# Performance work log

Measured on AMD Instinct MI355X. Metric: run time of the kernel, lower is better.

## Reference

```python
import jax, jax.numpy as jnp
import numpy as np

B, C_IN, C_OUT, H, W, K = 8, 64, 64, 128, 128, 3
KK = K * K


def _conv(x, w, b):
    # 3x3, stride 1, padding 1 (matches nn.Conv2d(stride=1, padding=1))
    y = jax.lax.conv_general_dilated(
        x, w, window_strides=(1, 1), padding=((1, 1), (1, 1)),
        dimension_numbers=('NCHW', 'OIHW', 'NCHW'))
    return y + b[None, :, None, None]


def setup_inputs() -> dict:
    key = jax.random.key(0)
    k1, k2, k3, k4, k5 = jax.random.split(key, 5)
    x = jax.random.normal(k1, (B, C_IN, H, W), jnp.float32)
    s = 1.0 / np.sqrt(C_IN * K * K)  # torch conv default init range
    w_off = jax.random.uniform(k2, (2 * KK, C_IN, K, K), jnp.float32, -s, s)
    b_off = jax.random.uniform(k3, (2 * KK,), jnp.float32, -s, s)
    w_reg = jax.random.uniform(k4, (C_OUT, C_IN, K, K), jnp.float32, -s, s)
    b_reg = jax.random.uniform(k5, (C_OUT,), jnp.float32, -s, s)
    return {"x": x, "w_off": w_off, "b_off": b_off, "w_reg": w_reg, "b_reg": b_reg}


def _deform_sample(x, offsets):
    # Equivalent of the K*K grid_sample(align_corners=True, padding_mode='zeros')
    # loop + sum over kernel positions. The norm/unnorm cancel, so sampling is
    # at absolute pixel coords base_grid + offsets.
    B_, C, H_, W_ = x.shape
    off = offsets.reshape(B_, KK, 2, H_, W_).transpose(0, 3, 4, 1, 2)  # B,H,W,KK,2
    xs = off[..., 0] + jnp.arange(W_, dtype=x.dtype)[None, None, :, None]
    ys = off[..., 1] + jnp.arange(H_, dtype=x.dtype)[None, :, None, None]
    x0 = jnp.floor(xs)
    y0 = jnp.floor(ys)
    wx1 = xs - x0
    wx0 = 1.0 - wx1
    wy1 = ys - y0
    wy0 = 1.0 - wy1
    x_flat = x.reshape(B_, C, H_ * W_)

    def gather(yi, xi, w):
        valid = (xi >= 0) & (xi < W_) & (yi >= 0) & (yi < H_)  # zeros padding
        xi_c = jnp.clip(xi, 0, W_ - 1).astype(jnp.int32)
        yi_c = jnp.clip(yi, 0, H_ - 1).astype(jnp.int32)
        idx = (yi_c * W_ + xi_c).reshape(B_, 1, H_ * W_ * KK)
        g = jnp.take_along_axis(
            x_flat, jnp.broadcast_to(idx, (B_, C, H_ * W_ * KK)), axis=2)
        g = g.reshape(B_, C, H_, W_, KK)
        wm = (w * valid.astype(x.dtype))[:, None]  # B,1,H,W,KK
        return (g * wm).sum(-1)  # sum over the KK kernel positions

    return (gather(y0, x0, wy0 * wx0)
            + gather(y0, x0 + 1.0, wy0 * wx1)
            + gather(y0 + 1.0, x0, wy1 * wx0)
            + gather(y0 + 1.0, x0 + 1.0, wy1 * wx1))


def reference(x, w_off, b_off, w_reg, b_reg):
    offsets = _conv(x, w_off, b_off)          # B, 2*KK, H, W
    sampled = _deform_sample(x, offsets)      # B, C, H, W (summed over KK)
    return _conv(sampled, w_reg, b_reg)       # B, C_OUT, H, W
```

## Files before the change

kernel.cpp:

```cpp
#include <hip/hip_runtime.h>

#define B_ 8
#define CIN 64
#define COUT 64
#define H_ 128
#define W_ 128
#define HW (H_*W_)
#define OFFP 24

typedef __attribute__((ext_vector_type(8))) short short8;
typedef __attribute__((ext_vector_type(4))) short s16x4;
typedef __attribute__((ext_vector_type(4))) float f32x4;

__device__ __forceinline__ short f2bf(float f) {
    unsigned u = __float_as_uint(f);
    unsigned r = (u + 0x7fffu + ((u >> 16) & 1u)) >> 16;
    return (short)r;
}
__device__ __forceinline__ float bf2f(short s) {
    return __uint_as_float(((unsigned)(unsigned short)s) << 16);
}

template<int NT>
__device__ __forceinline__ void prep_one(const float* __restrict__ w, short* __restrict__ o,
                                         int i, int n_used) {
    int j = i & 7, lane = (i >> 3) & 63, rest = i >> 9;
    int nt = rest % NT, dc = rest / NT, c = dc & 1, d = dc >> 1;
    int oc = nt * 16 + (lane & 15);
    int ic = c * 32 + (lane >> 4) * 8 + j;
    float v = (oc < n_used) ? w[(oc * 64 + ic) * 9 + d] : 0.f;
    o[i] = f2bf(v);
}

__global__ __launch_bounds__(256) void k_tr(const float* __restrict__ x,
                                            short* __restrict__ xt,
                                            const float* __restrict__ wof,
                                            const float* __restrict__ wrg,
                                            short* __restrict__ wt1,
                                            short* __restrict__ wt2) {
    int i = blockIdx.x * 256 + threadIdx.x;
    if (i < 9 * 2 * 2 * 512) prep_one<2>(wof, wt1, i, 18);
    if (i < 9 * 2 * 4 * 512) prep_one<4>(wrg, wt2, i, 64);

    __shared__ float tile[64 * 129];
    int bh = blockIdx.x;
    int bb = bh & 7, h = bh >> 3;
    const float* xp = x + (size_t)bb * (CIN * HW) + h * W_;
#pragma unroll
    for (int j = 0; j < 32; ++j) {
        int e = threadIdx.x + 256 * j;
        int cc = e >> 7, ww = e & 127;
        tile[cc * 129 + ww] = __builtin_nontemporal_load(xp + cc * HW + ww);
    }
    __syncthreads();
    short* op = xt + (((size_t)(bb << 7) + h) << 13);
#pragma unroll
    for (int j = 0; j < 4; ++j) {
        int t = threadIdx.x + 256 * j;
        int ww = t >> 3, c0 = (t & 7) << 3;
        short8 o;
#pragma unroll
        for (int k = 0; k < 8; ++k) o[k] = f2bf(tile[(c0 + k) * 129 + ww]);
        *(short8*)(op + ww * 64 + c0) = o;
    }
}

__device__ __forceinline__ void stage4(short* A, const short* __restrict__ src,
                                       int bb, int h0, int tid) {
    int wv = tid >> 6, l = tid & 63;
    int r = wv >> 1, half = wv & 1;
    int y = h0 - 1 + r;
    int P0 = 1 + half * 64;
    int px0 = P0 + (l >> 3);
    int ckl = l & 7;
    if ((unsigned)y < H_) {
        int ckg = ckl ^ (px0 & 7);
        const short* gp = src + ((((size_t)(bb << 7) + y) << 7) + (px0 - 1)) * 64 + ckg * 8;
#pragma unroll
        for (int i = 0; i < 8; ++i) {
            short* lp = &A[(r * 130 + P0 + i * 8) * 64];
            __builtin_amdgcn_global_load_lds(
                (const __attribute__((address_space(1))) void*)(gp + i * 512),
                (__attribute__((address_space(3))) void*)lp, 16, 0, 0);
        }
    } else {
        short8 z = {0, 0, 0, 0, 0, 0, 0, 0};
#pragma unroll
        for (int i = 0; i < 8; ++i)
            *(short8*)(&A[(r * 130 + P0 + i * 8) * 64 + l * 8]) = z;
    }
    if (tid < 64) {
        int rr = tid >> 4, side = (tid >> 3) & 1, ck = tid & 7;
        int px = side * 129;
        short8 z = {0, 0, 0, 0, 0, 0, 0, 0};
        *(short8*)(&A[(rr * 130 + px) * 64 + ((ck ^ (px & 7)) << 3)]) = z;
    }
}

__device__ __forceinline__ void prep_task(int t, int h0,
                                          const unsigned short* __restrict__ St,
                                          s16x4* __restrict__ idxs,
                                          f32x4* __restrict__ wgs) {
    int pxl = (int)((unsigned)t / 9u);
    int tap = t - pxl * 9;
    int row = pxl >> 7, sx = pxl & 127;
    unsigned owk = *(const unsigned*)(St + pxl * OFFP + tap * 2);
    float ox = bf2f((short)(owk & 0xffff));
    float oy = bf2f((short)(owk >> 16));
    float xs = (float)sx + ox, ys = (float)(h0 + row) + oy;
    float x0f = floorf(xs), y0f = floorf(ys);
    float wx1 = xs - x0f, wx0 = 1.f - wx1;
    float wy1 = ys - y0f, wy0 = 1.f - wy1;
    int x0 = (int)x0f, y0 = (int)y0f;
    int x1 = x0 + 1, y1 = y0 + 1;
    int x0c = min(max(x0, 0), W_ - 1), x1c = min(max(x1, 0), W_ - 1);
    int y0c = min(max(y0, 0), H_ - 1), y1c = min(max(y1, 0), H_ - 1);
    bool vx0 = ((unsigned)x0 < W_), vx1 = ((unsigned)x1 < W_);
    bool vy0 = ((unsigned)y0 < H_), vy1 = ((unsigned)y1 < H_);
    f32x4 wg;
    wg[0] = (vy0 && vx0) ? wy0 * wx0 : 0.f;
    wg[1] = (vy0 && vx1) ? wy0 * wx1 : 0.f;
    wg[2] = (vy1 && vx0) ? wy1 * wx0 : 0.f;
    wg[3] = (vy1 && vx1) ? wy1 * wx1 : 0.f;
    s16x4 id;
    id[0] = (short)(y0c * W_ + x0c);
    id[1] = (short)(y0c * W_ + x1c);
    id[2] = (short)(y1c * W_ + x0c);
    id[3] = (short)(y1c * W_ + x1c);
    idxs[t] = id;
    wgs[t] = wg;
}

__global__ __launch_bounds__(512, 4) void k_c1s(const short* __restrict__ xt,
                                                const short* __restrict__ wt1,
                                                const float* __restrict__ bof,
                                                short* __restrict__ smp) {
    __shared__ __align__(16) short lds[33280 + 6144];
    short* A = lds;
    unsigned short* St = (unsigned short*)(lds + 33280);
    int blk = blockIdx.x, tid = threadIdx.x;
    int bb = blk & 7;
    int h0 = (blk >> 3) << 1;

    stage4(A, xt, bb, h0, tid);
    __syncthreads();

    int lane = tid & 63;
    int wave = tid >> 6;
    int lr = wave >> 2;
    int p0 = (wave & 3) * 32;
    int m = lane & 15, quad = lane >> 4;

    {
        f32x4 acc[2][2];
#pragma unroll
        for (int nt = 0; nt < 2; ++nt) {
            int oc = nt * 16 + m;
            float bv = (oc < 18) ? bof[oc] : 0.f;
#pragma unroll
            for (int mt = 0; mt < 2; ++mt) {
                acc[mt][nt][0] = bv; acc[mt][nt][1] = bv;
                acc[mt][nt][2] = bv; acc[mt][nt][3] = bv;
            }
        }
#pragma unroll
        for (int d = 0; d < 9; ++d) {
            int dy = d / 3, dx = d % 3;
#pragma unroll
            for (int c = 0; c < 2; ++c) {
                short8 a[2];
#pragma unroll
                for (int mt = 0; mt < 2; ++mt) {
                    int px = p0 + mt * 16 + m + dx;
                    a[mt] = *(const short8*)(&A[((lr + dy) * 130 + px) * 64 + (((c * 4 + quad) ^ (px & 7)) << 3)]);
                }
#pragma unroll
                for (int nt = 0; nt < 2; ++nt) {
                    short8 b = *(const short8*)(wt1 + ((((d * 2 + c) * 2 + nt) * 64 + lane) << 3));
#pragma unroll
                    for (int mt = 0; mt < 2; ++mt)
                        acc[mt][nt] = __builtin_amdgcn_mfma_f32_16x16x32_bf16(a[mt], b, acc[mt][nt], 0, 0, 0);
                }
            }
        }
#pragma unroll
        for (int nt = 0; nt < 2; ++nt) {
            int oc = nt * 16 + m;
            if (oc < 18) {
#pragma unroll
                for (int mt = 0; mt < 2; ++mt) {
                    int pl = lr * 128 + p0 + mt * 16 + quad * 4;
#pragma unroll
                    for (int r = 0; r < 4; ++r)
                        St[(pl + r) * OFFP + oc] = (unsigned short)f2bf(acc[mt][nt][r]);
                }
            }
        }
    }
    __syncthreads();

    s16x4* idxs = (s16x4*)lds;
    f32x4*  wgs  = (f32x4*)(lds + 9216);
    {
#pragma unroll
        for (int k = 0; k < 4; ++k) prep_task(tid + 512 * k, h0, St, idxs, wgs);
        if (tid < 256) prep_task(2048 + tid, h0, St, idxs, wgs);
    }
    __syncthreads();

    {
        int ck = tid & 7, sxb = tid >> 3;
        int cko = ck * 8;
        const short* xim = xt + ((size_t)bb << 20);
#pragma unroll
        for (int row = 0; row < 2; ++row) {
            int y = h0 + row;
#pragma unroll
            for (int hf = 0; hf < 2; ++hf) {
                int sx = sxb + hf * 64;
                int pb = (row * 128 + sx) * 9;
                float acc[8];
#pragma unroll
                for (int i = 0; i < 8; ++i) acc[i] = 0.f;
#pragma unroll
                for (int g = 0; g < 3; ++g) {
                    int eo[12]; float wf[12]; short8 v[12];
#pragma unroll
                    for (int t2 = 0; t2 < 3; ++t2) {
                        s16x4 id = idxs[pb + g * 3 + t2];
                        f32x4 wv = wgs[pb + g * 3 + t2];
#pragma unroll
                        for (int c = 0; c < 4; ++c) {
                            eo[t2 * 4 + c] = (((int)id[c]) << 6) + cko;
                            wf[t2 * 4 + c] = wv[c];
                        }
                    }
#pragma unroll
                    for (int n = 0; n < 12; ++n) v[n] = *(const short8*)(xim + eo[n]);
#pragma unroll
                    for (int n = 0; n < 12; ++n) {
                        float wvv = wf[n];
#pragma unroll
                        for (int i = 0; i < 8; ++i) acc[i] += wvv * bf2f(v[n][i]);
                    }
                }
                short8 o;
#pragma unroll
                for (int i = 0; i < 8; ++i) o[i] = f2bf(acc[i]);
                *(short8*)(smp + ((((size_t)(bb << 7) + y) << 7) + sx) * 64 + cko) = o;
            }
        }
    }
}

__global__ __launch_bounds__(512, 4) void k_conv2(const short* __restrict__ smp,
                                                  const short* __restrict__ wt2,
                                                  const float* __restrict__ brg,
                                                  float* __restrict__ out) {
    __shared__ __align__(16) short A[4 * 130 * 64];
    int blk = blockIdx.x, tid = threadIdx.x;
    int bb = blk & 7;
    int h0 = (blk >> 3) << 1;

    stage4(A, smp, bb, h0, tid);
    __syncthreads();

    int lane = tid & 63;
    int wave = tid >> 6;
    int lr = wave >> 2;
    int p0 = (wave & 3) * 32;
    int m = lane & 15, quad = lane >> 4;

    f32x4 acc[2][4];
#pragma unroll
    for (int nt = 0; nt < 4; ++nt) {
        float bv = brg[nt * 16 + m];
#pragma unroll
        for (int mt = 0; mt < 2; ++mt) {
            acc[mt][nt][0] = bv; acc[mt][nt][1] = bv;
            acc[mt][nt][2] = bv; acc[mt][nt][3] = bv;
        }
    }
#pragma unroll
    for (int d = 0; d < 9; ++d) {
        int dy = d / 3, dx = d % 3;
#pragma unroll
        for (int c = 0; c < 2; ++c) {
            short8 a[2];
#pragma unroll
            for (int mt = 0; mt < 2; ++mt) {
                int px = p0 + mt * 16 + m + dx;
                a[mt] = *(const short8*)(&A[((lr + dy) * 130 + px) * 64 + (((c * 4 + quad) ^ (px & 7)) << 3)]);
            }
#pragma unroll
            for (int nt = 0; nt < 4; ++nt) {
                short8 b = *(const short8*)(wt2 + ((((d * 2 + c) * 4 + nt) * 64 + lane) << 3));
#pragma unroll
                for (int mt = 0; mt < 2; ++mt)
                    acc[mt][nt] = __builtin_amdgcn_mfma_f32_16x16x32_bf16(a[mt], b, acc[mt][nt], 0, 0, 0);
            }
        }
    }
#pragma unroll
    for (int nt = 0; nt < 4; ++nt) {
        int oc = nt * 16 + m;
#pragma unroll
        for (int mt = 0; mt < 2; ++mt) {
            int wpix = p0 + mt * 16 + quad * 4;
            __builtin_nontemporal_store(acc[mt][nt],
                (f32x4*)(out + (((size_t)(bb * 64 + oc)) << 14) + ((h0 + lr) << 7) + wpix));
        }
    }
}

extern "C" void kernel_launch(void* const* d_in, const int* in_sizes, int n_in,
                              void* d_out, int out_size, void* d_ws, size_t ws_size,
                              hipStream_t stream) {
    const float* x   = (const float*)d_in[0];
    const float* wof = (const float*)d_in[1];
    const float* bof = (const float*)d_in[2];
    const float* wrg = (const float*)d_in[3];
    const float* brg = (const float*)d_in[4];
    float* out = (float*)d_out;

    char* ws = (char*)d_ws;
    short* xt  = (short*)ws;
    short* smp = (short*)(ws + 16777216);
    short* wt1 = (short*)(ws + 2 * 16777216);
    short* wt2 = (short*)(ws + 2 * 16777216 + 36864);

    k_tr   <<<dim3(B_ * H_),     256, 0, stream>>>(x, xt, wof, wrg, wt1, wt2);
    k_c1s  <<<dim3(B_ * H_ / 2), 512, 0, stream>>>(xt, wt1, bof, smp);
    k_conv2<<<dim3(B_ * H_ / 2), 512, 0, stream>>>(smp, wt2, brg, out);
}
```

Measured before the change: 143.4 us.

## Fuse deformable sampling and second conv via neighbor-block flag sync; use packed FMA

Merges the sampling kernel and the second convolution into one kernel. Each block publishes a release flag once its sampled rows are written and spin-waits on the flags of the blocks holding the adjacent row pairs before staging its halo. This removes one launch and the tail/drain gap between kernels. It relies on all 512 blocks being co-resident, which launch bounds of 4 blocks per CU should allow, and includes a guard counter against deadlock. The bilinear accumulation also now uses v_pk_fma_f32 on bf16 pairs unpacked from dwords, to halve the FMA instruction count.

```diff
diff --git a/kernel.cpp b/kernel.cpp
--- a/kernel.cpp
+++ b/kernel.cpp
@@ -11,6 +11,7 @@
 typedef __attribute__((ext_vector_type(8))) short short8;
 typedef __attribute__((ext_vector_type(4))) short s16x4;
 typedef __attribute__((ext_vector_type(4))) float f32x4;
+typedef __attribute__((ext_vector_type(2))) float f32x2;
 
 __device__ __forceinline__ short f2bf(float f) {
     unsigned u = __float_as_uint(f);
@@ -37,10 +38,12 @@
                                             const float* __restrict__ wof,
                                             const float* __restrict__ wrg,
                                             short* __restrict__ wt1,
-                                            short* __restrict__ wt2) {
+                                            short* __restrict__ wt2,
+                                            int* __restrict__ flags) {
     int i = blockIdx.x * 256 + threadIdx.x;
     if (i < 9 * 2 * 2 * 512) prep_one<2>(wof, wt1, i, 18);
     if (i < 9 * 2 * 4 * 512) prep_one<4>(wrg, wt2, i, 64);
+    if (i < 512) flags[i] = 0;
 
     __shared__ float tile[64 * 129];
     int bh = blockIdx.x;
@@ -131,10 +134,14 @@
     wgs[t] = wg;
 }
 
-__global__ __launch_bounds__(512, 4) void k_c1s(const short* __restrict__ xt,
-                                                const short* __restrict__ wt1,
-                                                const float* __restrict__ bof,
-                                                short* __restrict__ smp) {
+__global__ __launch_bounds__(512, 4) void k_main(const short* __restrict__ xt,
+                                                 const short* __restrict__ wt1,
+                                                 const short* __restrict__ wt2,
+                                                 const float* __restrict__ bof,
+                                                 const float* __restrict__ brg,
+                                                 short* __restrict__ smp,
+                                                 float* __restrict__ out,
+                                                 int* __restrict__ flags) {
     __shared__ __align__(16) short lds[33280 + 6144];
     short* A = lds;
     unsigned short* St = (unsigned short*)(lds + 33280);
@@ -200,7 +207,7 @@
     __syncthreads();
 
     s16x4* idxs = (s16x4*)lds;
-    f32x4*  wgs  = (f32x4*)(lds + 9216);
+    f32x4* wgs  = (f32x4*)(lds + 9216);
     {
 #pragma unroll
         for (int k = 0; k < 4; ++k) prep_task(tid + 512 * k, h0, St, idxs, wgs);
@@ -211,7 +218,7 @@
     {
         int ck = tid & 7, sxb = tid >> 3;
         int cko = ck * 8;
-        const short* xim = xt + ((size_t)bb << 20);
+        const short* ximc = xt + ((size_t)bb << 20) + cko;
 #pragma unroll
         for (int row = 0; row < 2; ++row) {
             int y = h0 + row;
@@ -219,9 +226,9 @@
             for (int hf = 0; hf < 2; ++hf) {
                 int sx = sxb + hf * 64;
                 int pb = (row * 128 + sx) * 9;
-                float acc[8];
-#pragma unroll
-                for (int i = 0; i < 8; ++i) acc[i] = 0.f;
+                f32x2 acc2[4];
+#pragma unroll
+                for (int q = 0; q < 4; ++q) { acc2[q][0] = 0.f; acc2[q][1] = 0.f; }
 #pragma unroll
                 for (int g = 0; g < 3; ++g) {
                     int eo[12]; float wf[12]; short8 v[12];
@@ -231,84 +238,93 @@
                         f32x4 wv = wgs[pb + g * 3 + t2];
 #pragma unroll
                         for (int c = 0; c < 4; ++c) {
-                            eo[t2 * 4 + c] = (((int)id[c]) << 6) + cko;
+                            eo[t2 * 4 + c] = ((int)id[c]) << 6;
                             wf[t2 * 4 + c] = wv[c];
                         }
                     }
 #pragma unroll
-                    for (int n = 0; n < 12; ++n) v[n] = *(const short8*)(xim + eo[n]);
+                    for (int n = 0; n < 12; ++n) v[n] = *(const short8*)(ximc + eo[n]);
 #pragma unroll
                     for (int n = 0; n < 12; ++n) {
                         float wvv = wf[n];
-#pragma unroll
-                        for (int i = 0; i < 8; ++i) acc[i] += wvv * bf2f(v[n][i]);
+                        f32x2 wp; wp[0] = wvv; wp[1] = wvv;
+                        const unsigned* vd = (const unsigned*)&v[n];
+#pragma unroll
+                        for (int q = 0; q < 4; ++q) {
+                            unsigned dwd = vd[q];
+                            f32x2 av;
+                            av[0] = __uint_as_float(dwd << 16);
+                            av[1] = __uint_as_float(dwd & 0xffff0000u);
+                            asm("v_pk_fma_f32 %0, %1, %2, %0" : "+v"(acc2[q]) : "v"(av), "v"(wp));
+                        }
                     }
                 }
                 short8 o;
 #pragma unroll
-                for (int i = 0; i < 8; ++i) o[i] = f2bf(acc[i]);
+                for (int i = 0; i < 8; ++i) o[i] = f2bf(acc2[i >> 1][i & 1]);
                 *(short8*)(smp + ((((size_t)(bb << 7) + y) << 7) + sx) * 64 + cko) = o;
             }
         }
     }
-}
-
-__global__ __launch_bounds__(512, 4) void k_conv2(const short* __restrict__ smp,
-                                                  const short* __restrict__ wt2,
-                                                  const float* __restrict__ brg,
-                                                  float* __restrict__ out) {
-    __shared__ __align__(16) short A[4 * 130 * 64];
-    int blk = blockIdx.x, tid = threadIdx.x;
-    int bb = blk & 7;
-    int h0 = (blk >> 3) << 1;
+
+    __threadfence();
+    __syncthreads();
+    if (tid == 0)
+        __hip_atomic_store(&flags[blk], 1, __ATOMIC_RELEASE, __HIP_MEMORY_SCOPE_AGENT);
+    if (tid < 2) {
+        int nb = blk + (tid ? 8 : -8);
+        if ((unsigned)nb < 512u) {
+            int guard = 0;
+            while (__hip_atomic_load(&flags[nb], __ATOMIC_ACQUIRE, __HIP_MEMORY_SCOPE_AGENT) == 0) {
+                __builtin_amdgcn_s_sleep(8);
+                if (++guard > (1 << 28)) break;
+            }
+        }
+    }
+    __syncthreads();
 
     stage4(A, smp, bb, h0, tid);
     __syncthreads();
-
-    int lane = tid & 63;
-    int wave = tid >> 6;
-    int lr = wave >> 2;
-    int p0 = (wave & 3) * 32;
-    int m = lane & 15, quad = lane >> 4;
-
-    f32x4 acc[2][4];
-#pragma unroll
-    for (int nt = 0; nt < 4; ++nt) {
-        float bv = brg[nt * 16 + m];
-#pragma unroll
-        for (int mt = 0; mt < 2; ++mt) {
-            acc[mt][nt][0] = bv; acc[mt][nt][1] = bv;
-            acc[mt][nt][2] = bv; acc[mt][nt][3] = bv;
-        }
-    }
-#pragma unroll
-    for (int d = 0; d < 9; ++d) {
-        int dy = d / 3, dx = d % 3;
-#pragma unroll
-        for (int c = 0; c < 2; ++c) {
-            short8 a[2];
+    {
+        f32x4 acc[2][4];
+#pragma unroll
+        for (int nt = 0; nt < 4; ++nt) {
+            float bv = brg[nt * 16 + m];
 #pragma unroll
             for (int mt = 0; mt < 2; ++mt) {
-                int px = p0 + mt * 16 + m + dx;
-                a[mt] = *(const short8*)(&A[((lr + dy) * 130 + px) * 64 + (((c * 4 + quad) ^ (px & 7)) << 3)]);
-            }
-#pragma unroll
-            for (int nt = 0; nt < 4; ++nt) {
-                short8 b = *(const short8*)(wt2 + ((((d * 2 + c) * 4 + nt) * 64 + lane) << 3));
-#pragma unroll
-                for (int mt = 0; mt < 2; ++mt)
-                    acc[mt][nt] = __builtin_amdgcn_mfma_f32_16x16x32_bf16(a[mt], b, acc[mt][nt], 0, 0, 0);
-            }
-        }
-    }
-#pragma unroll
-    for (int nt = 0; nt < 4; ++nt) {
-        int oc = nt * 16 + m;
-#pragma unroll
-        for (int mt = 0; mt < 2; ++mt) {
-            int wpix = p0 + mt * 16 + quad * 4;
-            __builtin_nontemporal_store(acc[mt][nt],
-                (f32x4*)(out + (((size_t)(bb * 64 + oc)) << 14) + ((h0 + lr) << 7) + wpix));
+                acc[mt][nt][0] = bv; acc[mt][nt][1] = bv;
+                acc[mt][nt][2] = bv; acc[mt][nt][3] = bv;
+            }
+        }
+#pragma unroll
+        for (int d = 0; d < 9; ++d) {
+            int dy = d / 3, dx = d % 3;
+#pragma unroll
+            for (int c = 0; c < 2; ++c) {
+                short8 a[2];
+#pragma unroll
+                for (int mt = 0; mt < 2; ++mt) {
+                    int px = p0 + mt * 16 + m + dx;
+                    a[mt] = *(const short8*)(&A[((lr + dy) * 130 + px) * 64 + (((c * 4 + quad) ^ (px & 7)) << 3)]);
+                }
+#pragma unroll
+                for (int nt = 0; nt < 4; ++nt) {
+                    short8 b = *(const short8*)(wt2 + ((((d * 2 + c) * 4 + nt) * 64 + lane) << 3));
+#pragma unroll
+                    for (int mt = 0; mt < 2; ++mt)
+                        acc[mt][nt] = __builtin_amdgcn_mfma_f32_16x16x32_bf16(a[mt], b, acc[mt][nt], 0, 0, 0);
+                }
+            }
+        }
+#pragma unroll
+        for (int nt = 0; nt < 4; ++nt) {
+            int oc = nt * 16 + m;
+#pragma unroll
+            for (int mt = 0; mt < 2; ++mt) {
+                int wpix = p0 + mt * 16 + quad * 4;
+                __builtin_nontemporal_store(acc[mt][nt],
+                    (f32x4*)(out + (((size_t)(bb * 64 + oc)) << 14) + ((h0 + lr) << 7) + wpix));
+            }
         }
     }
 }
@@ -328,8 +344,8 @@
     short* smp = (short*)(ws + 16777216);
     short* wt1 = (short*)(ws + 2 * 16777216);
     short* wt2 = (short*)(ws + 2 * 16777216 + 36864);
-
-    k_tr   <<<dim3(B_ * H_),     256, 0, stream>>>(x, xt, wof, wrg, wt1, wt2);
-    k_c1s  <<<dim3(B_ * H_ / 2), 512, 0, stream>>>(xt, wt1, bof, smp);
-    k_conv2<<<dim3(B_ * H_ / 2), 512, 0, stream>>>(smp, wt2, brg, out);
-}
+    int* flags = (int*)(ws + 2 * 16777216 + 36864 + 73728);
+
+    k_tr  <<<dim3(B_ * H_),     256, 0, stream>>>(x, xt, wof, wrg, wt1, wt2, flags);
+    k_main<<<dim3(B_ * H_ / 2), 512, 0, stream>>>(xt, wt1, wt2, bof, brg, smp, out, flags);
+}
```

Result: slower. 267.0 us (+86.2%).

## Split offset conv and deformable sampling into separate kernels with 2D sample tiles

Applied to the files above, without the earlier changes.

The fused offset-conv plus sampling kernel is split in two. The offset conv now writes bf16 offsets to a global buffer. A new sampling kernel runs 256-thread blocks over 8x4 pixel tiles, so gather locality improves and occupancy rises because the large LDS staging buffer is gone. The bilinear accumulation uses packed v_pk_fma_f32 through inline asm. The cost is an extra kernel launch and a global round trip for the offsets, about 12MB of buffer space.

```diff
diff --git a/kernel.cpp b/kernel.cpp
--- a/kernel.cpp
+++ b/kernel.cpp
@@ -11,6 +11,7 @@
 typedef __attribute__((ext_vector_type(8))) short short8;
 typedef __attribute__((ext_vector_type(4))) short s16x4;
 typedef __attribute__((ext_vector_type(4))) float f32x4;
+typedef __attribute__((ext_vector_type(2))) float f32x2;
 
 __device__ __forceinline__ short f2bf(float f) {
     unsigned u = __float_as_uint(f);
@@ -97,17 +98,90 @@
     }
 }
 
-__device__ __forceinline__ void prep_task(int t, int h0,
-                                          const unsigned short* __restrict__ St,
-                                          s16x4* __restrict__ idxs,
-                                          f32x4* __restrict__ wgs) {
-    int pxl = (int)((unsigned)t / 9u);
-    int tap = t - pxl * 9;
-    int row = pxl >> 7, sx = pxl & 127;
-    unsigned owk = *(const unsigned*)(St + pxl * OFFP + tap * 2);
+__global__ __launch_bounds__(512, 4) void k_c1(const short* __restrict__ xt,
+                                               const short* __restrict__ wt1,
+                                               const float* __restrict__ bof,
+                                               short* __restrict__ offb) {
+    __shared__ __align__(16) short lds[33280 + 6144];
+    short* A = lds;
+    unsigned short* St = (unsigned short*)(lds + 33280);
+    int blk = blockIdx.x, tid = threadIdx.x;
+    int bb = blk & 7;
+    int h0 = (blk >> 3) << 1;
+
+    stage4(A, xt, bb, h0, tid);
+    __syncthreads();
+
+    int lane = tid & 63;
+    int wave = tid >> 6;
+    int lr = wave >> 2;
+    int p0 = (wave & 3) * 32;
+    int m = lane & 15, quad = lane >> 4;
+
+    f32x4 acc[2][2];
+#pragma unroll
+    for (int nt = 0; nt < 2; ++nt) {
+        int oc = nt * 16 + m;
+        float bv = (oc < 18) ? bof[oc] : 0.f;
+#pragma unroll
+        for (int mt = 0; mt < 2; ++mt) {
+            acc[mt][nt][0] = bv; acc[mt][nt][1] = bv;
+            acc[mt][nt][2] = bv; acc[mt][nt][3] = bv;
+        }
+    }
+#pragma unroll
+    for (int d = 0; d < 9; ++d) {
+        int dy = d / 3, dx = d % 3;
+#pragma unroll
+        for (int c = 0; c < 2; ++c) {
+            short8 a[2];
+#pragma unroll
+            for (int mt = 0; mt < 2; ++mt) {
+                int px = p0 + mt * 16 + m + dx;
+                a[mt] = *(const short8*)(&A[((lr + dy) * 130 + px) * 64 + (((c * 4 + quad) ^ (px & 7)) << 3)]);
+            }
+#pragma unroll
+            for (int nt = 0; nt < 2; ++nt) {
+                short8 b = *(const short8*)(wt1 + ((((d * 2 + c) * 2 + nt) * 64 + lane) << 3));
+#pragma unroll
+                for (int mt = 0; mt < 2; ++mt)
+                    acc[mt][nt] = __builtin_amdgcn_mfma_f32_16x16x32_bf16(a[mt], b, acc[mt][nt], 0, 0, 0);
+            }
+        }
+    }
+#pragma unroll
+    for (int nt = 0; nt < 2; ++nt) {
+        int oc = nt * 16 + m;
+        if (oc < 18) {
+#pragma unroll
+            for (int mt = 0; mt < 2; ++mt) {
+                int pl = lr * 128 + p0 + mt * 16 + quad * 4;
+#pragma unroll
+                for (int r = 0; r < 4; ++r)
+                    St[(pl + r) * OFFP + oc] = (unsigned short)f2bf(acc[mt][nt][r]);
+            }
+        }
+    }
+    __syncthreads();
+    const unsigned* Sd = (const unsigned*)St;
+    unsigned* Od = (unsigned*)(offb + ((size_t)((bb << 14) + (h0 << 7))) * OFFP);
+#pragma unroll
+    for (int j = 0; j < 6; ++j)
+        Od[tid + 512 * j] = Sd[tid + 512 * j];
+}
+
+__device__ __forceinline__ void prep_task_s(int t, int tw, int th,
+                                            const unsigned* __restrict__ sow,
+                                            s16x4* __restrict__ idxs,
+                                            f32x4* __restrict__ wgs) {
+    int px = (int)((unsigned)t / 9u);
+    int tap = t - px * 9;
+    int row = px >> 3, sx8 = px & 7;
+    unsigned owk = sow[row * 96 + sx8 * 12 + tap];
     float ox = bf2f((short)(owk & 0xffff));
     float oy = bf2f((short)(owk >> 16));
-    float xs = (float)sx + ox, ys = (float)(h0 + row) + oy;
+    float xs = (float)((tw << 3) + sx8) + ox;
+    float ys = (float)((th << 2) + row) + oy;
     float x0f = floorf(xs), y0f = floorf(ys);
     float wx1 = xs - x0f, wx0 = 1.f - wx1;
     float wy1 = ys - y0f, wy0 = 1.f - wy1;
@@ -131,126 +205,73 @@
     wgs[t] = wg;
 }
 
-__global__ __launch_bounds__(512, 4) void k_c1s(const short* __restrict__ xt,
-                                                const short* __restrict__ wt1,
-                                                const float* __restrict__ bof,
-                                                short* __restrict__ smp) {
-    __shared__ __align__(16) short lds[33280 + 6144];
-    short* A = lds;
-    unsigned short* St = (unsigned short*)(lds + 33280);
+__global__ __launch_bounds__(256, 4) void k_samp(const short* __restrict__ xt,
+                                                 const short* __restrict__ offb,
+                                                 short* __restrict__ smp) {
+    __shared__ unsigned sow[4 * 96];
+    __shared__ s16x4 idxs[288];
+    __shared__ f32x4 wgs[288];
     int blk = blockIdx.x, tid = threadIdx.x;
     int bb = blk & 7;
-    int h0 = (blk >> 3) << 1;
-
-    stage4(A, xt, bb, h0, tid);
-    __syncthreads();
-
-    int lane = tid & 63;
-    int wave = tid >> 6;
-    int lr = wave >> 2;
-    int p0 = (wave & 3) * 32;
-    int m = lane & 15, quad = lane >> 4;
+    int tile = blk >> 3;
+    int tw = tile & 15, th = tile >> 4;
 
     {
-        f32x4 acc[2][2];
-#pragma unroll
-        for (int nt = 0; nt < 2; ++nt) {
-            int oc = nt * 16 + m;
-            float bv = (oc < 18) ? bof[oc] : 0.f;
-#pragma unroll
-            for (int mt = 0; mt < 2; ++mt) {
-                acc[mt][nt][0] = bv; acc[mt][nt][1] = bv;
-                acc[mt][nt][2] = bv; acc[mt][nt][3] = bv;
-            }
-        }
-#pragma unroll
-        for (int d = 0; d < 9; ++d) {
-            int dy = d / 3, dx = d % 3;
-#pragma unroll
-            for (int c = 0; c < 2; ++c) {
-                short8 a[2];
-#pragma unroll
-                for (int mt = 0; mt < 2; ++mt) {
-                    int px = p0 + mt * 16 + m + dx;
-                    a[mt] = *(const short8*)(&A[((lr + dy) * 130 + px) * 64 + (((c * 4 + quad) ^ (px & 7)) << 3)]);
-                }
-#pragma unroll
-                for (int nt = 0; nt < 2; ++nt) {
-                    short8 b = *(const short8*)(wt1 + ((((d * 2 + c) * 2 + nt) * 64 + lane) << 3));
-#pragma unroll
-                    for (int mt = 0; mt < 2; ++mt)
-                        acc[mt][nt] = __builtin_amdgcn_mfma_f32_16x16x32_bf16(a[mt], b, acc[mt][nt], 0, 0, 0);
-                }
-            }
-        }
-#pragma unroll
-        for (int nt = 0; nt < 2; ++nt) {
-            int oc = nt * 16 + m;
-            if (oc < 18) {
-#pragma unroll
-                for (int mt = 0; mt < 2; ++mt) {
-                    int pl = lr * 128 + p0 + mt * 16 + quad * 4;
-#pragma unroll
-                    for (int r = 0; r < 4; ++r)
-                        St[(pl + r) * OFFP + oc] = (unsigned short)f2bf(acc[mt][nt][r]);
-                }
-            }
-        }
-    }
-    __syncthreads();
-
-    s16x4* idxs = (s16x4*)lds;
-    f32x4*  wgs  = (f32x4*)(lds + 9216);
-    {
-#pragma unroll
-        for (int k = 0; k < 4; ++k) prep_task(tid + 512 * k, h0, St, idxs, wgs);
-        if (tid < 256) prep_task(2048 + tid, h0, St, idxs, wgs);
-    }
-    __syncthreads();
-
-    {
-        int ck = tid & 7, sxb = tid >> 3;
-        int cko = ck * 8;
-        const short* xim = xt + ((size_t)bb << 20);
-#pragma unroll
-        for (int row = 0; row < 2; ++row) {
-            int y = h0 + row;
-#pragma unroll
-            for (int hf = 0; hf < 2; ++hf) {
-                int sx = sxb + hf * 64;
-                int pb = (row * 128 + sx) * 9;
-                float acc[8];
-#pragma unroll
-                for (int i = 0; i < 8; ++i) acc[i] = 0.f;
-#pragma unroll
-                for (int g = 0; g < 3; ++g) {
-                    int eo[12]; float wf[12]; short8 v[12];
-#pragma unroll
-                    for (int t2 = 0; t2 < 3; ++t2) {
-                        s16x4 id = idxs[pb + g * 3 + t2];
-                        f32x4 wv = wgs[pb + g * 3 + t2];
-#pragma unroll
-                        for (int c = 0; c < 4; ++c) {
-                            eo[t2 * 4 + c] = (((int)id[c]) << 6) + cko;
-                            wf[t2 * 4 + c] = wv[c];
-                        }
-                    }
-#pragma unroll
-                    for (int n = 0; n < 12; ++n) v[n] = *(const short8*)(xim + eo[n]);
-#pragma unroll
-                    for (int n = 0; n < 12; ++n) {
-                        float wvv = wf[n];
-#pragma unroll
-                        for (int i = 0; i < 8; ++i) acc[i] += wvv * bf2f(v[n][i]);
-                    }
-                }
-                short8 o;
-#pragma unroll
-                for (int i = 0; i < 8; ++i) o[i] = f2bf(acc[i]);
-                *(short8*)(smp + ((((size_t)(bb << 7) + y) << 7) + sx) * 64 + cko) = o;
-            }
-        }
-    }
+        int rowid = tid >> 6, rl = tid & 63;
+        const unsigned* srcp = (const unsigned*)(offb +
+            ((size_t)((bb << 14) + (((th << 2) + rowid) << 7) + (tw << 3))) * OFFP);
+        sow[rowid * 96 + rl] = __builtin_nontemporal_load(srcp + rl);
+        if (rl < 32) sow[rowid * 96 + 64 + rl] = __builtin_nontemporal_load(srcp + 64 + rl);
+    }
+    __syncthreads();
+
+    prep_task_s(tid, tw, th, sow, idxs, wgs);
+    if (tid < 32) prep_task_s(tid + 256, tw, th, sow, idxs, wgs);
+    __syncthreads();
+
+    int lp = tid >> 3, ck = tid & 7, cko = ck * 8;
+    int w = (tw << 3) + (lp & 7);
+    int h = (th << 2) + (lp >> 3);
+    const short* ximc = xt + ((size_t)bb << 20) + cko;
+    int pb = lp * 9;
+
+    f32x2 acc2[4];
+#pragma unroll
+    for (int q = 0; q < 4; ++q) { acc2[q][0] = 0.f; acc2[q][1] = 0.f; }
+#pragma unroll
+    for (int g = 0; g < 3; ++g) {
+        int eo[12]; float wf[12]; short8 v[12];
+#pragma unroll
+        for (int t2 = 0; t2 < 3; ++t2) {
+            s16x4 id = idxs[pb + g * 3 + t2];
+            f32x4 wv = wgs[pb + g * 3 + t2];
+#pragma unroll
+            for (int c = 0; c < 4; ++c) {
+                eo[t2 * 4 + c] = ((int)id[c]) << 6;
+                wf[t2 * 4 + c] = wv[c];
+            }
+        }
+#pragma unroll
+        for (int n = 0; n < 12; ++n) v[n] = *(const short8*)(ximc + eo[n]);
+#pragma unroll
+        for (int n = 0; n < 12; ++n) {
+            float wvv = wf[n];
+            f32x2 wp; wp[0] = wvv; wp[1] = wvv;
+            const unsigned* vd = (const unsigned*)&v[n];
+#pragma unroll
+            for (int q = 0; q < 4; ++q) {
+                unsigned dwd = vd[q];
+                f32x2 av;
+                av[0] = __uint_as_float(dwd << 16);
+                av[1] = __uint_as_float(dwd & 0xffff0000u);
+                asm("v_pk_fma_f32 %0, %1, %2, %0" : "+v"(acc2[q]) : "v"(av), "v"(wp));
+            }
+        }
+    }
+    short8 o;
+#pragma unroll
+    for (int i = 0; i < 8; ++i) o[i] = f2bf(acc2[i >> 1][i & 1]);
+    *(short8*)(smp + ((((size_t)(bb << 7) + h) << 7) + w) * 64 + cko) = o;
 }
 
 __global__ __launch_bounds__(512, 4) void k_conv2(const short* __restrict__ smp,
@@ -324,12 +345,14 @@
     float* out = (float*)d_out;
 
     char* ws = (char*)d_ws;
-    short* xt  = (short*)ws;
-    short* smp = (short*)(ws + 16777216);
-    short* wt1 = (short*)(ws + 2 * 16777216);
-    short* wt2 = (short*)(ws + 2 * 16777216 + 36864);
-
-    k_tr   <<<dim3(B_ * H_),     256, 0, stream>>>(x, xt, wof, wrg, wt1, wt2);
-    k_c1s  <<<dim3(B_ * H_ / 2), 512, 0, stream>>>(xt, wt1, bof, smp);
-    k_conv2<<<dim3(B_ * H_ / 2), 512, 0, stream>>>(smp, wt2, brg, out);
-}
+    short* xt   = (short*)ws;
+    short* smp  = (short*)(ws + 16777216);
+    short* offb = (short*)(ws + 2 * 16777216);
+    short* wt1  = (short*)(ws + 2 * 16777216 + 12582912);
+    short* wt2  = (short*)(ws + 2 * 16777216 + 12582912 + 36864);
+
+    k_tr   <<<dim3(B_ * H_),           256, 0, stream>>>(x, xt, wof, wrg, wt1, wt2);
+    k_c1   <<<dim3(B_ * H_ / 2),       512, 0, stream>>>(xt, wt1, bof, offb);
+    k_samp <<<dim3((B_ * HW) / 32),    256, 0, stream>>>(xt, offb, smp);
+    k_conv2<<<dim3(B_ * H_ / 2),       512, 0, stream>>>(smp, wt2, brg, out);
+}
```

After: 144.3 us. Within noise of the previous version (+0.6%).
